# Kernel tuning notes

Hardware: AMD Instinct MI355X
Metric: run time of the kernel (lower is better)

## Reference

```python
import jax, jax.numpy as jnp
import numpy as np

B, T, D, M, L = 4, 2048, 256, 128, 16
P = M * L  # max_pair_cnt


def setup_inputs() -> dict:
    key = jax.random.key(0)
    ks = jax.random.split(key, 11)
    head = jax.random.normal(ks[0], (B, P, T), jnp.float32) * 0.05
    tail = jax.random.normal(ks[1], (B, P, T), jnp.float32) * 0.05
    x = jax.random.normal(ks[2], (B, T, D), jnp.float32)
    coref_mention_position = jax.random.uniform(ks[3], (B, M, T), jnp.float32)
    lab = jax.random.uniform(ks[4], (B, P, 2), jnp.float32) + 1e-3
    coref_label = lab / lab.sum(-1, keepdims=True)  # already-softmaxed target
    coref_label_mask = jax.random.randint(ks[5], (B, P), 0, 2).astype(bool)
    lens = jnp.full((B, M), L, jnp.int32)  # uniform segment lengths
    w1 = jax.random.normal(ks[6], (3 * D, D), jnp.float32) / np.sqrt(3 * D).astype(np.float32)
    b1 = jnp.zeros((D,), jnp.float32)
    w2 = jax.random.normal(ks[7], (D, 2), jnp.float32) / np.sqrt(D).astype(np.float32)
    b2 = jnp.zeros((2,), jnp.float32)
    return {"head": head, "tail": tail, "lens": lens, "x": x,
            "coref_mention_position": coref_mention_position,
            "coref_label": coref_label, "coref_label_mask": coref_label_mask,
            "w1": w1, "b1": b1, "w2": w2, "b2": b2}


def reference(head, tail, lens, x, coref_mention_position, coref_label,
              coref_label_mask, w1, b1, w2, b2):
    # bmm-based gather of mention reps: [B,P,T] @ [B,T,D] -> [B,P,D]
    head_rep = jnp.einsum('bpt,btd->bpd', head, x)
    tail_rep = jnp.einsum('bpt,btd->bpd', tail, x)
    feat = jnp.concatenate([head_rep, tail_rep, head_rep * tail_rep], axis=-1)
    logits = jax.nn.relu(feat @ w1 + b1) @ w2 + b2  # [B,P,2]

    # ragged split_n_pad -> per-mention top-1 select (uniform lens == L -> reshape)
    scores = logits[..., 1].reshape(B, M, L)            # [B,M,L]
    max_idx = jnp.argmax(scores, axis=-1)               # [B,M]
    max_val = jnp.max(scores, axis=-1)                  # [B,M] (raw logit, as in source)
    tail_seg = tail_rep.reshape(B, M, L, D)
    sel = jnp.take_along_axis(tail_seg, max_idx[:, :, None, None], axis=2)[:, :, 0, :]
    coref_rep_m = sel * max_val[:, :, None]             # [B,M,D]

    # scatter-bmm merge back into sequence: [B,T,M] @ [B,M,D] -> [B,T,D]
    coref_rep = jnp.einsum('bmt,bmd->btd', coref_mention_position, coref_rep_m)
    output = x + coref_rep

    # KLDivLoss(reduction='mean') over masked pairs
    logq = jax.nn.log_softmax(logits, axis=-1)
    lab = coref_label
    pw = jnp.where(lab > 0, lab * jnp.log(jnp.maximum(lab, 1e-38)), 0.0) - lab * logq
    n = jnp.sum(coref_label_mask).astype(jnp.float32)
    loss = jnp.where(coref_label_mask[..., None], pw, 0.0).sum() / (n * 2.0)
    return output, loss
```

## Files before the change

kernel.cpp:

```cpp
#include <hip/hip_runtime.h>
#include <hip/hip_bf16.h>
#include <stdint.h>

#define TAU 0.05f

typedef __attribute__((ext_vector_type(8))) _Float16 f16x8;
typedef __attribute__((ext_vector_type(4))) float f32x4;

__device__ __forceinline__ unsigned short f2h(float f) {
  _Float16 h = (_Float16)f;
  return __builtin_bit_cast(unsigned short, h);
}
__device__ __forceinline__ void async_copy16(const void* g, void* l) {
  __builtin_amdgcn_global_load_lds(
      (const __attribute__((address_space(1))) unsigned int*)g,
      (__attribute__((address_space(3))) unsigned int*)l, 16, 0, 0);
}

__global__ __launch_bounds__(256) void k_prep(
    const float* __restrict__ x, const float* __restrict__ w1,
    const float* __restrict__ b2,
    unsigned short* __restrict__ xt, unsigned short* __restrict__ w1t,
    float* __restrict__ logits, int* __restrict__ njobs) {
  __shared__ float tileS[64][65];
  int bx = blockIdx.x, tid = threadIdx.x;
  if (bx == 0 && tid == 0) *njobs = 0;
  if (bx < 64) {
    int i = bx * 256 + tid;
    logits[i] = b2[i & 1];
  }
  int j = tid & 63, i0 = tid >> 6;
  if (bx < 512) {
    int b = bx >> 7, t6 = (bx >> 2) & 31, d6 = bx & 3;
    const float* src = x + ((size_t)b * 2048 + (size_t)t6 * 64) * 256 + d6 * 64;
    for (int i = i0; i < 64; i += 4) tileS[i][j] = src[(size_t)i * 256 + j];
    __syncthreads();
    unsigned short* dst = xt + ((size_t)b * 256 + (size_t)d6 * 64) * 2048 + t6 * 64;
    for (int r = i0; r < 64; r += 4) dst[(size_t)r * 2048 + j] = f2h(tileS[j][r]);
  } else {
    int wt = bx - 512;
    int k6 = wt >> 2, n6 = wt & 3;
    const float* src = w1 + ((size_t)k6 * 64) * 256 + n6 * 64;
    for (int i = i0; i < 64; i += 4) tileS[i][j] = src[(size_t)i * 256 + j];
    __syncthreads();
    unsigned short* dst = w1t + ((size_t)n6 * 64) * 768 + k6 * 64;
    for (int r = i0; r < 64; r += 4) dst[(size_t)r * 768 + j] = f2h(tileS[j][r]);
  }
}

__global__ __launch_bounds__(256, 4) void k_gemm_rep(
    const float* __restrict__ head, const float* __restrict__ tail,
    const unsigned short* __restrict__ xt,
    float* __restrict__ hrep, float* __restrict__ trep) {
  __shared__ unsigned short As[2][4096];
  __shared__ unsigned short Bs[2][4096];
  int bx = blockIdx.x;
  int ntile = bx >> 8;
  int g = bx & 255;
  int b = g >> 6, mtile = g & 63;
  const float* Asrc = ((mtile < 32) ? head : tail) +
                      ((size_t)(b * 2048 + (mtile & 31) * 64)) * 2048;
  float* Crep = (mtile < 32) ? hrep : trep;
  const unsigned short* Bsrc = xt + ((size_t)(b * 256 + ntile * 64)) * 2048;

  int tid = threadIdx.x, lane = tid & 63, w = tid >> 6;
  int l15 = lane & 15, l4 = lane >> 4;

  const float* aptr = Asrc + (size_t)(w * 16 + l15) * 2048 + l4 * 16;
  int aw_chunk0 = (l4 * 2) * 64 + w * 16 + l15;
  int aw_chunk1 = (l4 * 2 + 1) * 64 + w * 16 + l15;

  const unsigned short* bg0 = Bsrc + (size_t)lane * 2048 + 2 * w * 8;
  const unsigned short* bg1 = bg0 + 8;

  int ac0 = ((0 + l4) * 64 + w * 16 + l15) * 8;
  int ac1 = ((4 + l4) * 64 + w * 16 + l15) * 8;
  int bc[2][4];
#pragma unroll
  for (int kh = 0; kh < 2; ++kh)
#pragma unroll
    for (int ct = 0; ct < 4; ++ct)
      bc[kh][ct] = ((kh * 4 + l4) * 64 + ct * 16 + l15) * 8;

  f32x4 acc[4];
#pragma unroll
  for (int ct = 0; ct < 4; ++ct) acc[ct] = (f32x4){0.f, 0.f, 0.f, 0.f};

  auto pack_write = [&](float4* av, unsigned short* Abuf) {
    f16x8 p0, p1;
    p0[0] = (_Float16)av[0].x; p0[1] = (_Float16)av[0].y;
    p0[2] = (_Float16)av[0].z; p0[3] = (_Float16)av[0].w;
    p0[4] = (_Float16)av[1].x; p0[5] = (_Float16)av[1].y;
    p0[6] = (_Float16)av[1].z; p0[7] = (_Float16)av[1].w;
    p1[0] = (_Float16)av[2].x; p1[1] = (_Float16)av[2].y;
    p1[2] = (_Float16)av[2].z; p1[3] = (_Float16)av[2].w;
    p1[4] = (_Float16)av[3].x; p1[5] = (_Float16)av[3].y;
    p1[6] = (_Float16)av[3].z; p1[7] = (_Float16)av[3].w;
    *(f16x8*)&Abuf[aw_chunk0 * 8] = p0;
    *(f16x8*)&Abuf[aw_chunk1 * 8] = p1;
  };

  float4 avW[4], avF[4];
  {
    const float4* ap = (const float4*)aptr;
    avW[0] = ap[0]; avW[1] = ap[1]; avW[2] = ap[2]; avW[3] = ap[3];
  }
  async_copy16(bg0, &Bs[0][(2 * w * 64) * 8]);
  async_copy16(bg1, &Bs[0][((2 * w + 1) * 64) * 8]);
  pack_write(avW, As[0]);
  {
    const float4* ap = (const float4*)(aptr + 64);
    avW[0] = ap[0]; avW[1] = ap[1]; avW[2] = ap[2]; avW[3] = ap[3];
  }
  __syncthreads();

  for (int it = 0; it < 32; ++it) {
    int cur = it & 1, nxt = cur ^ 1;
    if (it < 31) {
      const unsigned short* g0 = Bsrc + (size_t)lane * 2048 + (it + 1) * 64 + 2 * w * 8;
      async_copy16(g0, &Bs[nxt][(2 * w * 64) * 8]);
      async_copy16(g0 + 8, &Bs[nxt][((2 * w + 1) * 64) * 8]);
    }
    if (it < 30) {
      const float4* ap = (const float4*)(aptr + (it + 2) * 64);
      avF[0] = ap[0]; avF[1] = ap[1]; avF[2] = ap[2]; avF[3] = ap[3];
    }
    const unsigned short* A_ = As[cur];
    const unsigned short* B_ = Bs[cur];
    f16x8 a0 = *(const f16x8*)&A_[ac0];
    f16x8 a1 = *(const f16x8*)&A_[ac1];
#pragma unroll
    for (int ct = 0; ct < 4; ++ct) {
      f16x8 b0 = *(const f16x8*)&B_[bc[0][ct]];
      acc[ct] = __builtin_amdgcn_mfma_f32_16x16x32_f16(a0, b0, acc[ct], 0, 0, 0);
    }
#pragma unroll
    for (int ct = 0; ct < 4; ++ct) {
      f16x8 b1 = *(const f16x8*)&B_[bc[1][ct]];
      acc[ct] = __builtin_amdgcn_mfma_f32_16x16x32_f16(a1, b1, acc[ct], 0, 0, 0);
    }
    if (it < 31) {
      pack_write(avW, As[nxt]);
      avW[0] = avF[0]; avW[1] = avF[1]; avW[2] = avF[2]; avW[3] = avF[3];
    }
    __syncthreads();
  }

  size_t prow = (size_t)b * 2048 + (size_t)(mtile & 31) * 64 + w * 16 + l4 * 4;
  int cb = ntile * 64 + l15;
#pragma unroll
  for (int ct = 0; ct < 4; ++ct)
#pragma unroll
    for (int i = 0; i < 4; ++i)
      Crep[(prow + i) * 256 + cb + ct * 16] = acc[ct][i];
}

__global__ __launch_bounds__(256) void k_feat(
    const float* __restrict__ hrep, const float* __restrict__ trep,
    unsigned short* __restrict__ featf) {
  int gid = blockIdx.x * 256 + threadIdx.x;
  int p = gid >> 6, d0 = (gid & 63) * 4;
  float4 h4 = *(const float4*)&hrep[(size_t)p * 256 + d0];
  float4 t4 = *(const float4*)&trep[(size_t)p * 256 + d0];
  ushort4 a, bb, c;
  a.x = f2h(h4.x); a.y = f2h(h4.y); a.z = f2h(h4.z); a.w = f2h(h4.w);
  bb.x = f2h(t4.x); bb.y = f2h(t4.y); bb.z = f2h(t4.z); bb.w = f2h(t4.w);
  c.x = f2h(h4.x * t4.x); c.y = f2h(h4.y * t4.y);
  c.z = f2h(h4.z * t4.z); c.w = f2h(h4.w * t4.w);
  *(ushort4*)&featf[(size_t)p * 768 + d0] = a;
  *(ushort4*)&featf[(size_t)p * 768 + 256 + d0] = bb;
  *(ushort4*)&featf[(size_t)p * 768 + 512 + d0] = c;
}

__global__ __launch_bounds__(256, 4) void k_gemm_mlp(
    const unsigned short* __restrict__ featf, const unsigned short* __restrict__ w1t,
    const float* __restrict__ b1, const float* __restrict__ w2,
    float* __restrict__ logits) {
  __shared__ unsigned short As[2][4096], Bs[2][4096];
  int bx = blockIdx.x;
  int ntile = bx >> 7;
  int mtile = bx & 127;
  int tid = threadIdx.x, lane = tid & 63, w = tid >> 6;
  int l15 = lane & 15, l4 = lane >> 4;

  const unsigned short* Ag = featf + (size_t)(mtile * 64 + lane) * 768 + 2 * w * 8;
  const unsigned short* Bg = w1t + (size_t)(ntile * 64 + lane) * 768 + 2 * w * 8;

  int ac0 = ((0 + l4) * 64 + w * 16 + l15) * 8;
  int ac1 = ((4 + l4) * 64 + w * 16 + l15) * 8;
  int bc[2][4];
#pragma unroll
  for (int kh = 0; kh < 2; ++kh)
#pragma unroll
    for (int ct = 0; ct < 4; ++ct)
      bc[kh][ct] = ((kh * 4 + l4) * 64 + ct * 16 + l15) * 8;

  f32x4 acc[4];
#pragma unroll
  for (int ct = 0; ct < 4; ++ct) acc[ct] = (f32x4){0.f, 0.f, 0.f, 0.f};

  async_copy16(Ag, &As[0][(2 * w * 64) * 8]);
  async_copy16(Ag + 8, &As[0][((2 * w + 1) * 64) * 8]);
  async_copy16(Bg, &Bs[0][(2 * w * 64) * 8]);
  async_copy16(Bg + 8, &Bs[0][((2 * w + 1) * 64) * 8]);
  __syncthreads();

  for (int it = 0; it < 12; ++it) {
    int cur = it & 1, nxt = cur ^ 1;
    if (it < 11) {
      const unsigned short* ga = Ag + (it + 1) * 64;
      const unsigned short* gb = Bg + (it + 1) * 64;
      async_copy16(ga, &As[nxt][(2 * w * 64) * 8]);
      async_copy16(ga + 8, &As[nxt][((2 * w + 1) * 64) * 8]);
      async_copy16(gb, &Bs[nxt][(2 * w * 64) * 8]);
      async_copy16(gb + 8, &Bs[nxt][((2 * w + 1) * 64) * 8]);
    }
    const unsigned short* A_ = As[cur];
    const unsigned short* B_ = Bs[cur];
    f16x8 a0 = *(const f16x8*)&A_[ac0];
    f16x8 a1 = *(const f16x8*)&A_[ac1];
#pragma unroll
    for (int ct = 0; ct < 4; ++ct) {
      f16x8 b0 = *(const f16x8*)&B_[bc[0][ct]];
      acc[ct] = __builtin_amdgcn_mfma_f32_16x16x32_f16(a0, b0, acc[ct], 0, 0, 0);
    }
#pragma unroll
    for (int ct = 0; ct < 4; ++ct) {
      f16x8 b1 = *(const f16x8*)&B_[bc[1][ct]];
      acc[ct] = __builtin_amdgcn_mfma_f32_16x16x32_f16(a1, b1, acc[ct], 0, 0, 0);
    }
    __syncthreads();
  }

  float bv[4], w20[4], w21[4];
#pragma unroll
  for (int ct = 0; ct < 4; ++ct) {
    int col = ntile * 64 + ct * 16 + l15;
    bv[ct] = b1[col]; w20[ct] = w2[col * 2]; w21[ct] = w2[col * 2 + 1];
  }
#pragma unroll
  for (int i = 0; i < 4; ++i) {
    float s0 = 0.f, s1 = 0.f;
#pragma unroll
    for (int ct = 0; ct < 4; ++ct) {
      float r = fmaxf(acc[ct][i] + bv[ct], 0.f);
      s0 += r * w20[ct]; s1 += r * w21[ct];
    }
#pragma unroll
    for (int off = 1; off < 16; off <<= 1) {
      s0 += __shfl_xor(s0, off); s1 += __shfl_xor(s1, off);
    }
    if (l15 == 0) {
      int row = mtile * 64 + w * 16 + l4 * 4 + i;
      atomicAdd(&logits[row * 2], s0);
      atomicAdd(&logits[row * 2 + 1], s1);
    }
  }
}

__global__ void k_select(const float* __restrict__ logits, int* __restrict__ idxv,
                         float* __restrict__ mval, int* __restrict__ cmask,
                         int* __restrict__ njobs, int* __restrict__ jobs) {
  int q = blockIdx.x * 256 + threadIdx.x;
  if (q >= 512) return;
  int base = q * 16;
  float s[16];
#pragma unroll
  for (int i = 0; i < 16; ++i) s[i] = logits[(size_t)(base + i) * 2 + 1];
  float best = s[0]; int bi = 0;
#pragma unroll
  for (int i = 1; i < 16; ++i) if (s[i] > best) { best = s[i]; bi = i; }
  int mask = 0, cnt = 0;
#pragma unroll
  for (int i = 0; i < 16; ++i) if (s[i] > best - TAU) { mask |= 1 << i; ++cnt; }
  idxv[q] = bi; mval[q] = best;
  if (cnt > 1) {
    cmask[q] = mask;
    for (int i = 0; i < 16; ++i)
      if ((mask >> i) & 1) { int j = atomicAdd(njobs, 1); jobs[j] = base + i; }
  } else cmask[q] = 0;
}

__global__ __launch_bounds__(1024) void k_refine(
    const int* __restrict__ njobs, const int* __restrict__ jobs,
    const float* __restrict__ head, const float* __restrict__ tail,
    const float* __restrict__ x, const float* __restrict__ w1,
    const float* __restrict__ b1, const float* __restrict__ w2,
    const float* __restrict__ b2, float* __restrict__ refined) {
  __shared__ float hrow[2048], trow[2048], feat[768], red[1024], red2[1024];
  int tid = threadIdx.x, seg = tid >> 8, d = tid & 255;
  int nj = *njobs;
  for (int job = blockIdx.x; job < nj; job += gridDim.x) {
    int code = jobs[job];
    int b = code >> 11, p = code & 2047;
    if (tid < 512)
      *(float4*)&hrow[tid * 4] = *(const float4*)&head[((size_t)(b * 2048 + p)) * 2048 + tid * 4];
    else {
      int u = tid - 512;
      *(float4*)&trow[u * 4] = *(const float4*)&tail[((size_t)(b * 2048 + p)) * 2048 + u * 4];
    }
    __syncthreads();
    float hr = 0.f, tr = 0.f;
    const float* xb = x + ((size_t)b * 2048) * 256 + d;
#pragma unroll 8
    for (int t = seg * 512; t < seg * 512 + 512; ++t) {
      float xv = xb[(size_t)t * 256];
      hr += hrow[t] * xv; tr += trow[t] * xv;
    }
    red[tid] = hr; red2[tid] = tr;
    __syncthreads();
    if (seg == 0) {
      float fh = red[d] + red[256 + d] + red[512 + d] + red[768 + d];
      float ft = red2[d] + red2[256 + d] + red2[512 + d] + red2[768 + d];
      feat[d] = fh; feat[256 + d] = ft; feat[512 + d] = fh * ft;
    }
    __syncthreads();
    float hp = 0.f;
    for (int ii = seg * 192; ii < seg * 192 + 192; ++ii) hp += feat[ii] * w1[(size_t)ii * 256 + d];
    red[tid] = hp;
    __syncthreads();
    if (seg == 0) {
      float hj = b1[d] + red[d] + red[256 + d] + red[512 + d] + red[768 + d];
      hj = fmaxf(hj, 0.f);
      red2[d] = hj * w2[d * 2 + 1];
    }
    __syncthreads();
    for (int s = 128; s > 0; s >>= 1) {
      if (tid < s) red2[tid] += red2[tid + s];
      __syncthreads();
    }
    if (tid == 0) refined[code] = red2[0] + b2[1];
    __syncthreads();
  }
}

__global__ __launch_bounds__(256) void k_repm(
    const int* __restrict__ idxv, const float* __restrict__ mval,
    const int* __restrict__ cmask, const float* __restrict__ refined,
    const float* __restrict__ trep, float* __restrict__ repm) {
  int q = blockIdx.x, d = threadIdx.x;
  int mask = cmask[q]; int bi; float v;
  if (mask) {
    bi = -1; v = -1e30f;
    for (int i = 0; i < 16; ++i)
      if ((mask >> i) & 1) { float s = refined[q * 16 + i]; if (s > v) { v = s; bi = i; } }
  } else { bi = idxv[q]; v = mval[q]; }
  repm[(size_t)q * 256 + d] = trep[((size_t)q * 16 + bi) * 256 + d] * v;
}

__global__ __launch_bounds__(256) void k_merge(
    const float* __restrict__ cmp, const float* __restrict__ repm,
    const float* __restrict__ x, float* __restrict__ out) {
  __shared__ float cl[128 * 16];
  int bx = blockIdx.x, b = bx >> 7, t0 = (bx & 127) * 16;
  int tid = threadIdx.x;
#pragma unroll
  for (int it = 0; it < 2; ++it) {
    int f = it * 256 + tid;
    int row = f >> 2, c4 = (f & 3) * 4;
    *(float4*)&cl[row * 16 + c4] =
        *(const float4*)&cmp[((size_t)(b * 128 + row)) * 2048 + t0 + c4];
  }
  __syncthreads();
  float acc[16];
#pragma unroll
  for (int i = 0; i < 16; ++i) acc[i] = 0.f;
  int d = tid;
  for (int m = 0; m < 128; ++m) {
    float rv = repm[(size_t)(b * 128 + m) * 256 + d];
    const float4* c4p = (const float4*)&cl[m * 16];
#pragma unroll
    for (int jj = 0; jj < 4; ++jj) {
      float4 c = c4p[jj];
      acc[jj * 4] += c.x * rv; acc[jj * 4 + 1] += c.y * rv;
      acc[jj * 4 + 2] += c.z * rv; acc[jj * 4 + 3] += c.w * rv;
    }
  }
  const float* xb = x + ((size_t)(b * 2048 + t0)) * 256 + d;
  float* ob = out + ((size_t)(b * 2048 + t0)) * 256 + d;
#pragma unroll
  for (int tt = 0; tt < 16; ++tt) ob[(size_t)tt * 256] = xb[(size_t)tt * 256] + acc[tt];
}

__global__ __launch_bounds__(1024) void k_loss(
    const float* __restrict__ logits, const float* __restrict__ lab,
    const unsigned char* __restrict__ mask, float* __restrict__ out_loss) {
  __shared__ float rs[1024], rc[1024];
  int tid = threadIdx.x;
  float sum = 0.f, cnt = 0.f;
  for (int p = tid; p < 8192; p += 1024) {
    float l0 = logits[(size_t)p * 2], l1 = logits[(size_t)p * 2 + 1];
    float a0 = lab[(size_t)p * 2], a1 = lab[(size_t)p * 2 + 1];
    float mx = fmaxf(l0, l1);
    float lse = mx + logf(expf(l0 - mx) + expf(l1 - mx));
    float pw = 0.f;
    if (a0 > 0.f) pw += a0 * logf(fmaxf(a0, 1e-38f));
    if (a1 > 0.f) pw += a1 * logf(fmaxf(a1, 1e-38f));
    pw -= a0 * (l0 - lse) + a1 * (l1 - lse);
    if (mask[p]) { sum += pw; cnt += 1.f; }
  }
  rs[tid] = sum; rc[tid] = cnt;
  __syncthreads();
  for (int s = 512; s > 0; s >>= 1) {
    if (tid < s) { rs[tid] += rs[tid + s]; rc[tid] += rc[tid + s]; }
    __syncthreads();
  }
  if (tid == 0) *out_loss = rs[0] / (rc[0] * 2.0f);
}

extern "C" void kernel_launch(void* const* d_in, const int* in_sizes, int n_in,
                              void* d_out, int out_size, void* d_ws, size_t ws_size,
                              hipStream_t stream) {
  (void)in_sizes; (void)n_in; (void)out_size; (void)ws_size;
  const float* head = (const float*)d_in[0];
  const float* tail = (const float*)d_in[1];
  const float* x = (const float*)d_in[3];
  const float* cmp = (const float*)d_in[4];
  const float* lab = (const float*)d_in[5];
  const unsigned char* lmask = (const unsigned char*)d_in[6];
  const float* w1 = (const float*)d_in[7];
  const float* b1 = (const float*)d_in[8];
  const float* w2 = (const float*)d_in[9];
  const float* b2 = (const float*)d_in[10];
  float* out = (float*)d_out;

  char* ws = (char*)d_ws;
  size_t off = 0;
  auto alloc = [&](size_t bytes) -> void* {
    void* p = ws + off; off += (bytes + 255) & ~(size_t)255; return p;
  };
  unsigned short* xt = (unsigned short*)alloc(4ull * 256 * 2048 * 2);
  unsigned short* w1t = (unsigned short*)alloc(256ull * 768 * 2);
  float* hrep = (float*)alloc(8192ull * 256 * 4);
  float* trep = (float*)alloc(8192ull * 256 * 4);
  unsigned short* featf = (unsigned short*)alloc(8192ull * 768 * 2);
  float* logits = (float*)alloc(8192ull * 2 * 4);
  float* refined = (float*)alloc(8192ull * 4);
  int* idxv = (int*)alloc(512 * 4);
  float* mvalv = (float*)alloc(512 * 4);
  int* cmaskv = (int*)alloc(512 * 4);
  int* njobs = (int*)alloc(256);
  int* jobs = (int*)alloc(8192 * 4);
  float* repm = (float*)alloc(512ull * 256 * 4);

  k_prep<<<560, 256, 0, stream>>>(x, w1, b2, xt, w1t, logits, njobs);
  k_gemm_rep<<<1024, 256, 0, stream>>>(head, tail, xt, hrep, trep);
  k_feat<<<2048, 256, 0, stream>>>(hrep, trep, featf);
  k_gemm_mlp<<<512, 256, 0, stream>>>(featf, w1t, b1, w2, logits);
  k_select<<<2, 256, 0, stream>>>(logits, idxv, mvalv, cmaskv, njobs, jobs);
  k_refine<<<256, 1024, 0, stream>>>(njobs, jobs, head, tail, x, w1, b1, w2, b2, refined);
  k_repm<<<512, 256, 0, stream>>>(idxv, mvalv, cmaskv, refined, trep, repm);
  k_merge<<<512, 256, 0, stream>>>(cmp, repm, x, out);
  k_loss<<<1, 1024, 0, stream>>>(logits, lab, lmask, out + 4ull * 2048 * 256);
}
```

Before: 334.6 us.

## Widen rep GEMM tile to full N and drop LDS staging in MLP GEMM

New measurement: 340.6 us. No clear change (+1.8%).

```diff
diff --git a/kernel.cpp b/kernel.cpp
--- a/kernel.cpp
+++ b/kernel.cpp
@@ -48,111 +48,87 @@
   }
 }
 
-__global__ __launch_bounds__(256, 4) void k_gemm_rep(
+__global__ __launch_bounds__(1024, 1) void k_gemm_rep(
     const float* __restrict__ head, const float* __restrict__ tail,
     const unsigned short* __restrict__ xt,
     float* __restrict__ hrep, float* __restrict__ trep) {
-  __shared__ unsigned short As[2][4096];
-  __shared__ unsigned short Bs[2][4096];
+  __shared__ unsigned short Bs[2][32768];
   int bx = blockIdx.x;
-  int ntile = bx >> 8;
-  int g = bx & 255;
-  int b = g >> 6, mtile = g & 63;
-  const float* Asrc = ((mtile < 32) ? head : tail) +
-                      ((size_t)(b * 2048 + (mtile & 31) * 64)) * 2048;
-  float* Crep = (mtile < 32) ? hrep : trep;
-  const unsigned short* Bsrc = xt + ((size_t)(b * 256 + ntile * 64)) * 2048;
+  int isTail = bx >> 7;
+  int g2 = bx & 127;
+  int b = g2 >> 5;
+  int rowt = (g2 & 31) * 64;
+  const float* Asrc = (isTail ? tail : head) + ((size_t)(b * 2048 + rowt)) * 2048;
+  float* Crep = isTail ? trep : hrep;
+  const unsigned short* xtb = xt + (size_t)b * 256 * 2048;
 
   int tid = threadIdx.x, lane = tid & 63, w = tid >> 6;
   int l15 = lane & 15, l4 = lane >> 4;
-
-  const float* aptr = Asrc + (size_t)(w * 16 + l15) * 2048 + l4 * 16;
-  int aw_chunk0 = (l4 * 2) * 64 + w * 16 + l15;
-  int aw_chunk1 = (l4 * 2 + 1) * 64 + w * 16 + l15;
-
-  const unsigned short* bg0 = Bsrc + (size_t)lane * 2048 + 2 * w * 8;
-  const unsigned short* bg1 = bg0 + 8;
-
-  int ac0 = ((0 + l4) * 64 + w * 16 + l15) * 8;
-  int ac1 = ((4 + l4) * 64 + w * 16 + l15) * 8;
-  int bc[2][4];
-#pragma unroll
-  for (int kh = 0; kh < 2; ++kh)
-#pragma unroll
-    for (int ct = 0; ct < 4; ++ct)
-      bc[kh][ct] = ((kh * 4 + l4) * 64 + ct * 16 + l15) * 8;
+  int msub = w & 3, nsub = w >> 2;
+  const float* rowptr = Asrc + (size_t)(msub * 16 + l15) * 2048 + l4 * 8;
 
   f32x4 acc[4];
 #pragma unroll
   for (int ct = 0; ct < 4; ++ct) acc[ct] = (f32x4){0.f, 0.f, 0.f, 0.f};
 
-  auto pack_write = [&](float4* av, unsigned short* Abuf) {
-    f16x8 p0, p1;
-    p0[0] = (_Float16)av[0].x; p0[1] = (_Float16)av[0].y;
-    p0[2] = (_Float16)av[0].z; p0[3] = (_Float16)av[0].w;
-    p0[4] = (_Float16)av[1].x; p0[5] = (_Float16)av[1].y;
-    p0[6] = (_Float16)av[1].z; p0[7] = (_Float16)av[1].w;
-    p1[0] = (_Float16)av[2].x; p1[1] = (_Float16)av[2].y;
-    p1[2] = (_Float16)av[2].z; p1[3] = (_Float16)av[2].w;
-    p1[4] = (_Float16)av[3].x; p1[5] = (_Float16)av[3].y;
-    p1[6] = (_Float16)av[3].z; p1[7] = (_Float16)av[3].w;
-    *(f16x8*)&Abuf[aw_chunk0 * 8] = p0;
-    *(f16x8*)&Abuf[aw_chunk1 * 8] = p1;
+  float4 aw[8], af[8];
+
+  auto stageB = [&](int iv, int buf) {
+    int k0 = iv * 128;
+#pragma unroll
+    for (int q = 0; q < 4; ++q) {
+      const unsigned short* src = xtb + (size_t)(q * 64 + lane) * 2048 + k0 + w * 8;
+      async_copy16(src, &Bs[buf][(w * 256 + q * 64 + lane) * 8]);
+    }
   };
-
-  float4 avW[4], avF[4];
-  {
-    const float4* ap = (const float4*)aptr;
-    avW[0] = ap[0]; avW[1] = ap[1]; avW[2] = ap[2]; avW[3] = ap[3];
-  }
-  async_copy16(bg0, &Bs[0][(2 * w * 64) * 8]);
-  async_copy16(bg1, &Bs[0][((2 * w + 1) * 64) * 8]);
-  pack_write(avW, As[0]);
-  {
-    const float4* ap = (const float4*)(aptr + 64);
-    avW[0] = ap[0]; avW[1] = ap[1]; avW[2] = ap[2]; avW[3] = ap[3];
-  }
+  auto loadA = [&](float4* dst, int iv) {
+    const float* p = rowptr + iv * 128;
+#pragma unroll
+    for (int s = 0; s < 4; ++s) {
+      dst[2 * s] = *(const float4*)(p + s * 32);
+      dst[2 * s + 1] = *(const float4*)(p + s * 32 + 4);
+    }
+  };
+
+  stageB(0, 0);
+  loadA(aw, 0);
   __syncthreads();
 
-  for (int it = 0; it < 32; ++it) {
-    int cur = it & 1, nxt = cur ^ 1;
-    if (it < 31) {
-      const unsigned short* g0 = Bsrc + (size_t)lane * 2048 + (it + 1) * 64 + 2 * w * 8;
-      async_copy16(g0, &Bs[nxt][(2 * w * 64) * 8]);
-      async_copy16(g0 + 8, &Bs[nxt][((2 * w + 1) * 64) * 8]);
-    }
-    if (it < 30) {
-      const float4* ap = (const float4*)(aptr + (it + 2) * 64);
-      avF[0] = ap[0]; avF[1] = ap[1]; avF[2] = ap[2]; avF[3] = ap[3];
-    }
-    const unsigned short* A_ = As[cur];
+  for (int iv = 0; iv < 16; ++iv) {
+    int cur = iv & 1, nxt = cur ^ 1;
+    if (iv < 15) {
+      stageB(iv + 1, nxt);
+      loadA(af, iv + 1);
+    }
     const unsigned short* B_ = Bs[cur];
-    f16x8 a0 = *(const f16x8*)&A_[ac0];
-    f16x8 a1 = *(const f16x8*)&A_[ac1];
-#pragma unroll
-    for (int ct = 0; ct < 4; ++ct) {
-      f16x8 b0 = *(const f16x8*)&B_[bc[0][ct]];
-      acc[ct] = __builtin_amdgcn_mfma_f32_16x16x32_f16(a0, b0, acc[ct], 0, 0, 0);
-    }
-#pragma unroll
-    for (int ct = 0; ct < 4; ++ct) {
-      f16x8 b1 = *(const f16x8*)&B_[bc[1][ct]];
-      acc[ct] = __builtin_amdgcn_mfma_f32_16x16x32_f16(a1, b1, acc[ct], 0, 0, 0);
-    }
-    if (it < 31) {
-      pack_write(avW, As[nxt]);
-      avW[0] = avF[0]; avW[1] = avF[1]; avW[2] = avF[2]; avW[3] = avF[3];
-    }
-    __syncthreads();
-  }
-
-  size_t prow = (size_t)b * 2048 + (size_t)(mtile & 31) * 64 + w * 16 + l4 * 4;
-  int cb = ntile * 64 + l15;
+#pragma unroll
+    for (int s = 0; s < 4; ++s) {
+      f16x8 a;
+      float4 u = aw[2 * s], v = aw[2 * s + 1];
+      a[0] = (_Float16)u.x; a[1] = (_Float16)u.y;
+      a[2] = (_Float16)u.z; a[3] = (_Float16)u.w;
+      a[4] = (_Float16)v.x; a[5] = (_Float16)v.y;
+      a[6] = (_Float16)v.z; a[7] = (_Float16)v.w;
+#pragma unroll
+      for (int ct = 0; ct < 4; ++ct) {
+        f16x8 bf = *(const f16x8*)&B_[((s * 4 + l4) * 256 + nsub * 64 + ct * 16 + l15) * 8];
+        acc[ct] = __builtin_amdgcn_mfma_f32_16x16x32_f16(a, bf, acc[ct], 0, 0, 0);
+      }
+    }
+    if (iv < 15) {
+#pragma unroll
+      for (int r = 0; r < 8; ++r) aw[r] = af[r];
+    }
+    __syncthreads();
+  }
+
+  size_t grow = (size_t)b * 2048 + rowt + msub * 16 + l4 * 4;
+  int gcol = nsub * 64 + l15;
 #pragma unroll
   for (int ct = 0; ct < 4; ++ct)
 #pragma unroll
     for (int i = 0; i < 4; ++i)
-      Crep[(prow + i) * 256 + cb + ct * 16] = acc[ct][i];
+      Crep[(grow + i) * 256 + gcol + ct * 16] = acc[ct][i];
 }
 
 __global__ __launch_bounds__(256) void k_feat(
@@ -172,90 +148,81 @@
   *(ushort4*)&featf[(size_t)p * 768 + 512 + d0] = c;
 }
 
-__global__ __launch_bounds__(256, 4) void k_gemm_mlp(
+__global__ __launch_bounds__(256) void k_gemm_mlp(
     const unsigned short* __restrict__ featf, const unsigned short* __restrict__ w1t,
     const float* __restrict__ b1, const float* __restrict__ w2,
     float* __restrict__ logits) {
-  __shared__ unsigned short As[2][4096], Bs[2][4096];
   int bx = blockIdx.x;
-  int ntile = bx >> 7;
-  int mtile = bx & 127;
+  int mt = bx >> 2, nt = bx & 3;
   int tid = threadIdx.x, lane = tid & 63, w = tid >> 6;
   int l15 = lane & 15, l4 = lane >> 4;
-
-  const unsigned short* Ag = featf + (size_t)(mtile * 64 + lane) * 768 + 2 * w * 8;
-  const unsigned short* Bg = w1t + (size_t)(ntile * 64 + lane) * 768 + 2 * w * 8;
-
-  int ac0 = ((0 + l4) * 64 + w * 16 + l15) * 8;
-  int ac1 = ((4 + l4) * 64 + w * 16 + l15) * 8;
-  int bc[2][4];
-#pragma unroll
-  for (int kh = 0; kh < 2; ++kh)
-#pragma unroll
-    for (int ct = 0; ct < 4; ++ct)
-      bc[kh][ct] = ((kh * 4 + l4) * 64 + ct * 16 + l15) * 8;
-
-  f32x4 acc[4];
-#pragma unroll
-  for (int ct = 0; ct < 4; ++ct) acc[ct] = (f32x4){0.f, 0.f, 0.f, 0.f};
-
-  async_copy16(Ag, &As[0][(2 * w * 64) * 8]);
-  async_copy16(Ag + 8, &As[0][((2 * w + 1) * 64) * 8]);
-  async_copy16(Bg, &Bs[0][(2 * w * 64) * 8]);
-  async_copy16(Bg + 8, &Bs[0][((2 * w + 1) * 64) * 8]);
-  __syncthreads();
-
-  for (int it = 0; it < 12; ++it) {
-    int cur = it & 1, nxt = cur ^ 1;
-    if (it < 11) {
-      const unsigned short* ga = Ag + (it + 1) * 64;
-      const unsigned short* gb = Bg + (it + 1) * 64;
-      async_copy16(ga, &As[nxt][(2 * w * 64) * 8]);
-      async_copy16(ga + 8, &As[nxt][((2 * w + 1) * 64) * 8]);
-      async_copy16(gb, &Bs[nxt][(2 * w * 64) * 8]);
-      async_copy16(gb + 8, &Bs[nxt][((2 * w + 1) * 64) * 8]);
-    }
-    const unsigned short* A_ = As[cur];
-    const unsigned short* B_ = Bs[cur];
-    f16x8 a0 = *(const f16x8*)&A_[ac0];
-    f16x8 a1 = *(const f16x8*)&A_[ac1];
-#pragma unroll
-    for (int ct = 0; ct < 4; ++ct) {
-      f16x8 b0 = *(const f16x8*)&B_[bc[0][ct]];
-      acc[ct] = __builtin_amdgcn_mfma_f32_16x16x32_f16(a0, b0, acc[ct], 0, 0, 0);
-    }
-#pragma unroll
-    for (int ct = 0; ct < 4; ++ct) {
-      f16x8 b1 = *(const f16x8*)&B_[bc[1][ct]];
-      acc[ct] = __builtin_amdgcn_mfma_f32_16x16x32_f16(a1, b1, acc[ct], 0, 0, 0);
-    }
-    __syncthreads();
-  }
-
-  float bv[4], w20[4], w21[4];
-#pragma unroll
-  for (int ct = 0; ct < 4; ++ct) {
-    int col = ntile * 64 + ct * 16 + l15;
-    bv[ct] = b1[col]; w20[ct] = w2[col * 2]; w21[ct] = w2[col * 2 + 1];
-  }
-#pragma unroll
-  for (int i = 0; i < 4; ++i) {
-    float s0 = 0.f, s1 = 0.f;
-#pragma unroll
-    for (int ct = 0; ct < 4; ++ct) {
-      float r = fmaxf(acc[ct][i] + bv[ct], 0.f);
-      s0 += r * w20[ct]; s1 += r * w21[ct];
-    }
-#pragma unroll
-    for (int off = 1; off < 16; off <<= 1) {
-      s0 += __shfl_xor(s0, off); s1 += __shfl_xor(s1, off);
-    }
-    if (l15 == 0) {
-      int row = mtile * 64 + w * 16 + l4 * 4 + i;
-      atomicAdd(&logits[row * 2], s0);
-      atomicAdd(&logits[row * 2 + 1], s1);
-    }
-  }
+  int wm = (w & 1) * 32, wn = (w >> 1) * 32;
+
+  const unsigned short* arow[2];
+  const unsigned short* brow[2];
+#pragma unroll
+  for (int j = 0; j < 2; ++j) {
+    arow[j] = featf + (size_t)(mt * 64 + wm + j * 16 + l15) * 768 + l4 * 8;
+    brow[j] = w1t + (size_t)(nt * 64 + wn + j * 16 + l15) * 768 + l4 * 8;
+  }
+
+  f32x4 acc[2][2];
+#pragma unroll
+  for (int jm = 0; jm < 2; ++jm)
+#pragma unroll
+    for (int jn = 0; jn < 2; ++jn) acc[jm][jn] = (f32x4){0.f, 0.f, 0.f, 0.f};
+
+  f16x8 a_[2][2], b_[2][2];
+#pragma unroll
+  for (int p = 0; p < 2; ++p)
+#pragma unroll
+    for (int j = 0; j < 2; ++j) {
+      a_[p][j] = *(const f16x8*)(arow[j] + p * 32);
+      b_[p][j] = *(const f16x8*)(brow[j] + p * 32);
+    }
+
+  for (int s = 0; s < 24; ++s) {
+    int c = s & 1;
+    f16x8 ta0 = a_[c][0], ta1 = a_[c][1], tb0 = b_[c][0], tb1 = b_[c][1];
+    if (s + 2 < 24) {
+#pragma unroll
+      for (int j = 0; j < 2; ++j) {
+        a_[c][j] = *(const f16x8*)(arow[j] + (s + 2) * 32);
+        b_[c][j] = *(const f16x8*)(brow[j] + (s + 2) * 32);
+      }
+    }
+    acc[0][0] = __builtin_amdgcn_mfma_f32_16x16x32_f16(ta0, tb0, acc[0][0], 0, 0, 0);
+    acc[0][1] = __builtin_amdgcn_mfma_f32_16x16x32_f16(ta0, tb1, acc[0][1], 0, 0, 0);
+    acc[1][0] = __builtin_amdgcn_mfma_f32_16x16x32_f16(ta1, tb0, acc[1][0], 0, 0, 0);
+    acc[1][1] = __builtin_amdgcn_mfma_f32_16x16x32_f16(ta1, tb1, acc[1][1], 0, 0, 0);
+  }
+
+  float bv[2], w20[2], w21[2];
+#pragma unroll
+  for (int jn = 0; jn < 2; ++jn) {
+    int col = nt * 64 + wn + jn * 16 + l15;
+    bv[jn] = b1[col]; w20[jn] = w2[col * 2]; w21[jn] = w2[col * 2 + 1];
+  }
+#pragma unroll
+  for (int jm = 0; jm < 2; ++jm)
+#pragma unroll
+    for (int i = 0; i < 4; ++i) {
+      float s0 = 0.f, s1 = 0.f;
+#pragma unroll
+      for (int jn = 0; jn < 2; ++jn) {
+        float r = fmaxf(acc[jm][jn][i] + bv[jn], 0.f);
+        s0 += r * w20[jn]; s1 += r * w21[jn];
+      }
+#pragma unroll
+      for (int off = 1; off < 16; off <<= 1) {
+        s0 += __shfl_xor(s0, off); s1 += __shfl_xor(s1, off);
+      }
+      if (l15 == 0) {
+        int row = mt * 64 + wm + jm * 16 + l4 * 4 + i;
+        atomicAdd(&logits[row * 2], s0);
+        atomicAdd(&logits[row * 2 + 1], s1);
+      }
+    }
 }
 
 __global__ void k_select(const float* __restrict__ logits, int* __restrict__ idxv,
@@ -444,7 +411,7 @@
   float* repm = (float*)alloc(512ull * 256 * 4);
 
   k_prep<<<560, 256, 0, stream>>>(x, w1, b2, xt, w1t, logits, njobs);
-  k_gemm_rep<<<1024, 256, 0, stream>>>(head, tail, xt, hrep, trep);
+  k_gemm_rep<<<256, 1024, 0, stream>>>(head, tail, xt, hrep, trep);
   k_feat<<<2048, 256, 0, stream>>>(hrep, trep, featf);
   k_gemm_mlp<<<512, 256, 0, stream>>>(featf, w1t, b1, w2, logits);
   k_select<<<2, 256, 0, stream>>>(logits, idxv, mvalv, cmaskv, njobs, jobs);
```
